# Kernel tuning notes

Measured on AMD Instinct MI355X. Metric: run time of the kernel, lower is better.

The kernel has to match this reference:

```python
import jax, jax.numpy as jnp
import numpy as np
from jax import lax

GAMMA = 1.0

def _conv(x, w, b, stride, pad):
    y = lax.conv_general_dilated(x, w, (stride, stride), [(pad, pad), (pad, pad)],
                                 dimension_numbers=('NCHW', 'OIHW', 'NCHW'))
    return y + b[None, :, None, None]

def _maxpool2s1(x):
    return lax.reduce_window(x, -jnp.inf, lax.max, (1, 1, 2, 2), (1, 1, 1, 1), 'VALID')

def setup_inputs() -> dict:
    key = jax.random.key(0)
    ks = jax.random.split(key, 13)
    d = {}
    d['x'] = jax.random.normal(ks[0], (128, 3, 250, 250), dtype=jnp.float32)
    d['conv1_w'] = jax.random.normal(ks[1], (6, 3, 5, 5), dtype=jnp.float32) / np.sqrt(3 * 25)
    d['conv1_b'] = jax.random.normal(ks[2], (6,), dtype=jnp.float32) * 0.01
    d['conv2_w'] = jax.random.normal(ks[3], (15, 6, 3, 3), dtype=jnp.float32) / np.sqrt(6 * 9)
    d['conv2_b'] = jax.random.normal(ks[4], (15,), dtype=jnp.float32) * 0.01
    d['fc1_w'] = jax.random.normal(ks[5], (120, 55815), dtype=jnp.float32) / np.sqrt(55815.0)
    d['fc1_b'] = jax.random.normal(ks[6], (120,), dtype=jnp.float32) * 0.01
    d['fc2_w'] = jax.random.normal(ks[7], (84, 120), dtype=jnp.float32) / np.sqrt(120.0)
    d['fc2_b'] = jax.random.normal(ks[8], (84,), dtype=jnp.float32) * 0.01
    d['fc3_w'] = jax.random.normal(ks[9], (1, 84), dtype=jnp.float32) / np.sqrt(84.0)
    d['fc3_b'] = jax.random.normal(ks[10], (1,), dtype=jnp.float32) * 0.01
    d['support'] = jax.random.normal(ks[11], (10, 1), dtype=jnp.float32)
    return d

def reference(x, conv1_w, conv1_b, conv2_w, conv2_b, fc1_w, fc1_b, fc2_w, fc2_b, fc3_w, fc3_b, support):
    h = jax.nn.relu(_conv(x, conv1_w, conv1_b, 2, 1))   # [B,6,124,124]
    h = _maxpool2s1(h)                                   # [B,6,123,123] (dropout = identity in eval)
    h = jax.nn.relu(_conv(h, conv2_w, conv2_b, 2, 1))    # [B,15,62,62]
    h = _maxpool2s1(h)                                   # [B,15,61,61]
    h = h.reshape(h.shape[0], -1)                        # [B,55815]
    h = jax.nn.relu(h @ fc1_w.T + fc1_b)
    h = jax.nn.relu(h @ fc2_w.T + fc2_b)
    h = h @ fc3_w.T + fc3_b                              # [B,1]
    # fused RBF kernel vs support set: k[i,j] = exp(-gamma*(x_i - s_j)^2)
    diff = h - support[:, 0][None, :]                    # [B,10]
    k = jnp.exp(-GAMMA * diff * diff)
    h = k.mean(axis=1, keepdims=True)                    # [B,1]
    probs = jax.nn.sigmoid(h)
    return jnp.concatenate((probs, 1.0 - probs), axis=-1)  # [B,2]
```

## Files before the change

### kernel.cpp

```cpp
#include <hip/hip_runtime.h>
#include <math.h>


#define BATCH 128

#define C1_ST 150
#define C1_TOT (37 * 133)
__global__ __launch_bounds__(256) void conv1_pool_kernel(
    const float* __restrict__ x, const float* __restrict__ w,
    const float* __restrict__ bias, float* __restrict__ out) {
  const int b = blockIdx.z;
  const int P0 = blockIdx.x * 64;
  const int R0 = blockIdx.y * 16;
  const int tid = threadIdx.x;
  const int t = tid >> 4;
  const int s = tid & 15;

  __shared__ float lds[37 * C1_ST];

  float acc0[5][6], acc1[5][6];
#pragma unroll
  for (int oc = 0; oc < 6; oc++) {
    float bv = bias[oc];
#pragma unroll
    for (int dc = 0; dc < 5; dc++) { acc0[dc][oc] = bv; acc1[dc][oc] = bv; }
  }

  const int ihb = 2 * R0 - 1, iwb = 2 * P0 - 1;

#pragma unroll 1
  for (int ci = 0; ci < 3; ci++) {
    __syncthreads();
    const float* src = x + (size_t)(b * 3 + ci) * 62500;
#pragma unroll 1
    for (int base = tid; base < C1_TOT; base += 2048) {
      float vv[8];
      int lrv[8], ilv[8];
#pragma unroll
      for (int k = 0; k < 8; k++) {
        int i = base + (k << 8);
        int lr = (int)(((unsigned)i * 63073u) >> 23);
        int il = i - lr * 133;
        lrv[k] = lr; ilv[k] = il;
        int ih = ihb + lr, iw = iwb + il;
        bool ok = (i < C1_TOT) && ((unsigned)ih < 250u) && ((unsigned)iw < 250u);
        vv[k] = ok ? src[ih * 250 + iw] : 0.f;
      }
#pragma unroll
      for (int k = 0; k < 8; k++) {
        int i = base + (k << 8);
        if (i < C1_TOT) lds[lrv[k] * C1_ST + ilv[k] + (ilv[k] >> 3)] = vv[k];
      }
    }
    __syncthreads();

#pragma unroll 1
    for (int ir = 0; ir < 7; ir++) {
      const float* rp = &lds[(2 * t + ir) * C1_ST + 9 * s];
      float v[13];
#pragma unroll
      for (int j = 0; j < 13; j++) v[j] = rp[j + (j >> 3)];

      if (ir < 5) {
#pragma unroll
        for (int oc = 0; oc < 6; oc++) {
          const float* wr = w + ((oc * 3 + ci) * 5 + ir) * 5;
          float w0 = wr[0], w1 = wr[1], w2 = wr[2], w3 = wr[3], w4 = wr[4];
#pragma unroll
          for (int dc = 0; dc < 5; dc++) {
            float a = acc0[dc][oc];
            a += w0 * v[2 * dc + 0];
            a += w1 * v[2 * dc + 1];
            a += w2 * v[2 * dc + 2];
            a += w3 * v[2 * dc + 3];
            a += w4 * v[2 * dc + 4];
            acc0[dc][oc] = a;
          }
        }
      }
      if (ir >= 2) {
#pragma unroll
        for (int oc = 0; oc < 6; oc++) {
          const float* wr = w + ((oc * 3 + ci) * 5 + (ir - 2)) * 5;
          float w0 = wr[0], w1 = wr[1], w2 = wr[2], w3 = wr[3], w4 = wr[4];
#pragma unroll
          for (int dc = 0; dc < 5; dc++) {
            float a = acc1[dc][oc];
            a += w0 * v[2 * dc + 0];
            a += w1 * v[2 * dc + 1];
            a += w2 * v[2 * dc + 2];
            a += w3 * v[2 * dc + 3];
            a += w4 * v[2 * dc + 4];
            acc1[dc][oc] = a;
          }
        }
      }
    }
  }

  const int r = R0 + t;
  const int c0 = P0 + 4 * s;
  if (r < 123) {
#pragma unroll
    for (int oc = 0; oc < 6; oc++) {
      float* orow = out + ((size_t)(b * 6 + oc) * 123 + r) * 123;
      float m0 = fmaxf(fmaxf(fmaxf(acc0[0][oc], acc0[1][oc]),
                             fmaxf(acc1[0][oc], acc1[1][oc])), 0.f);
      float m1 = fmaxf(fmaxf(fmaxf(acc0[1][oc], acc0[2][oc]),
                             fmaxf(acc1[1][oc], acc1[2][oc])), 0.f);
      float m2 = fmaxf(fmaxf(fmaxf(acc0[2][oc], acc0[3][oc]),
                             fmaxf(acc1[2][oc], acc1[3][oc])), 0.f);
      float m3 = fmaxf(fmaxf(fmaxf(acc0[3][oc], acc0[4][oc]),
                             fmaxf(acc1[3][oc], acc1[4][oc])), 0.f);
      if (c0 + 3 < 123) {
        float4 st = make_float4(m0, m1, m2, m3);
        *(float4*)&orow[c0] = st;
      } else {
        if (c0 < 123) orow[c0] = m0;
        if (c0 + 1 < 123) orow[c0 + 1] = m1;
        if (c0 + 2 < 123) orow[c0 + 2] = m2;
      }
    }
  }
}

#define C2_ST 84
#define C2_TOT (35 * 67)
__global__ __launch_bounds__(256) void conv2_pool_kernel(
    const float* __restrict__ in, const float* __restrict__ w,
    const float* __restrict__ bias, float* __restrict__ out) {
  const int b = blockIdx.z;
  const int P0 = blockIdx.x * 32;
  const int R0 = blockIdx.y * 16;
  const int tid = threadIdx.x;
  const int t = tid >> 4;
  const int s = tid & 15;

  __shared__ float lds[35 * C2_ST];

  const int ihb = 2 * R0 - 1, iwb = 2 * P0 - 1;
  const int r = R0 + t;
  const int c0 = P0 + 2 * s;

#pragma unroll 1
  for (int ocg = 0; ocg < 2; ocg++) {
    const int oc0 = ocg * 7;
    float acc0[3][8], acc1[3][8];
#pragma unroll
    for (int k = 0; k < 8; k++) {
      float bv = bias[oc0 + k];
#pragma unroll
      for (int dc = 0; dc < 3; dc++) { acc0[dc][k] = bv; acc1[dc][k] = bv; }
    }

#pragma unroll 1
    for (int ci = 0; ci < 6; ci++) {
      __syncthreads();
      const float* src = in + (size_t)(b * 6 + ci) * 15129;
#pragma unroll 1
      for (int base = tid; base < C2_TOT; base += 2048) {
        float vv[8];
        int lrv[8], ilv[8];
#pragma unroll
        for (int k = 0; k < 8; k++) {
          int i = base + (k << 8);
          int lr = (int)(((unsigned)i * 125204u) >> 23);
          int il = i - lr * 67;
          lrv[k] = lr; ilv[k] = il;
          int ih = ihb + lr, iw = iwb + il;
          bool ok = (i < C2_TOT) && ((unsigned)ih < 123u) && ((unsigned)iw < 123u);
          vv[k] = ok ? src[ih * 123 + iw] : 0.f;
        }
#pragma unroll
        for (int k = 0; k < 8; k++) {
          int i = base + (k << 8);
          if (i < C2_TOT) lds[lrv[k] * C2_ST + ilv[k] + (ilv[k] >> 2)] = vv[k];
        }
      }
      __syncthreads();

#pragma unroll 1
      for (int ir = 0; ir < 5; ir++) {
        const float* rp = &lds[(2 * t + ir) * C2_ST + 5 * s];
        float v[7];
#pragma unroll
        for (int j = 0; j < 7; j++) v[j] = rp[j + (j >> 2)];

        if (ir < 3) {
#pragma unroll
          for (int k = 0; k < 8; k++) {
            const float* wr = w + (((oc0 + k) * 6 + ci) * 3 + ir) * 3;
            float w0 = wr[0], w1 = wr[1], w2 = wr[2];
#pragma unroll
            for (int dc = 0; dc < 3; dc++) {
              float a = acc0[dc][k];
              a += w0 * v[2 * dc + 0];
              a += w1 * v[2 * dc + 1];
              a += w2 * v[2 * dc + 2];
              acc0[dc][k] = a;
            }
          }
        }
        if (ir >= 2) {
#pragma unroll
          for (int k = 0; k < 8; k++) {
            const float* wr = w + (((oc0 + k) * 6 + ci) * 3 + (ir - 2)) * 3;
            float w0 = wr[0], w1 = wr[1], w2 = wr[2];
#pragma unroll
            for (int dc = 0; dc < 3; dc++) {
              float a = acc1[dc][k];
              a += w0 * v[2 * dc + 0];
              a += w1 * v[2 * dc + 1];
              a += w2 * v[2 * dc + 2];
              acc1[dc][k] = a;
            }
          }
        }
      }
    }

    if (r < 61) {
#pragma unroll
      for (int k = 0; k < 8; k++) {
        int oc = oc0 + k;
        float* orow = out + ((size_t)(b * 15 + oc) * 61 + r) * 61;
        float m0 = fmaxf(fmaxf(fmaxf(acc0[0][k], acc0[1][k]),
                               fmaxf(acc1[0][k], acc1[1][k])), 0.f);
        float m1 = fmaxf(fmaxf(fmaxf(acc0[1][k], acc0[2][k]),
                               fmaxf(acc1[1][k], acc1[2][k])), 0.f);
        if (c0 + 1 < 61) {
          float2 st = make_float2(m0, m1);
          *(float2*)&orow[c0] = st;
        } else if (c0 < 61) {
          orow[c0] = m0;
        }
      }
    }
  }
}

#define KTOT 55815
#define NPART 512
#define KCHUNK 112
__global__ __launch_bounds__(512) void fc1_splitk_kernel(
    const float* __restrict__ act, const float* __restrict__ w,
    float* __restrict__ partial) {
  const int kbase = blockIdx.x * KCHUNK;
  const int tid = threadIdx.x;
  const int tx = tid & 31, ty = tid >> 5;
  __shared__ float ldsA[8 * 132];
  __shared__ float ldsB[8 * 132];
  float acc[8][4];
#pragma unroll
  for (int i = 0; i < 8; i++)
#pragma unroll
    for (int j = 0; j < 4; j++) acc[i][j] = 0.f;

  for (int s8 = 0; s8 < KCHUNK / 8; s8++) {
    int kofs = kbase + s8 * 8;
    __syncthreads();
    for (int i = tid; i < 1024; i += 512) {
      int m = i >> 3, kk = i & 7;
      int k = kofs + kk;
      ldsA[kk * 132 + m] = (k < KTOT) ? act[m * KTOT + k] : 0.f;
    }
    for (int i = tid; i < 960; i += 512) {
      int n = i >> 3, kk = i & 7;
      int k = kofs + kk;
      ldsB[kk * 132 + n] = (k < KTOT) ? w[n * KTOT + k] : 0.f;
    }
    __syncthreads();
#pragma unroll
    for (int kk = 0; kk < 8; kk++) {
      float4 a0 = *(const float4*)&ldsA[kk * 132 + ty * 8];
      float4 a1 = *(const float4*)&ldsA[kk * 132 + ty * 8 + 4];
      float4 b0 = *(const float4*)&ldsB[kk * 132 + tx * 4];
      float av[8] = {a0.x, a0.y, a0.z, a0.w, a1.x, a1.y, a1.z, a1.w};
      float bv[4] = {b0.x, b0.y, b0.z, b0.w};
#pragma unroll
      for (int i = 0; i < 8; i++)
#pragma unroll
        for (int j = 0; j < 4; j++) acc[i][j] += av[i] * bv[j];
    }
  }

  if (tx < 30) {
    float* dst = partial + (size_t)blockIdx.x * 15360;
#pragma unroll
    for (int i = 0; i < 8; i++) {
      int row = ty * 8 + i;
      float4 st = make_float4(acc[i][0], acc[i][1], acc[i][2], acc[i][3]);
      *(float4*)&dst[row * 120 + tx * 4] = st;
    }
  }
}

__global__ __launch_bounds__(64) void fc1_reduce1_kernel(
    const float* __restrict__ partial, float* __restrict__ partial2) {
  int idx = blockIdx.x * 64 + threadIdx.x;
  int g = blockIdx.y;
  const float* p = partial + (size_t)g * 64 * 15360 + idx;
  float s = 0.f;
#pragma unroll 8
  for (int q = 0; q < 64; q++) s += p[(size_t)q * 15360];
  partial2[(size_t)g * 15360 + idx] = s;
}

__global__ __launch_bounds__(64) void fc1_reduce2_kernel(
    const float* __restrict__ partial2, const float* __restrict__ bias,
    float* __restrict__ h1) {
  int idx = blockIdx.x * 64 + threadIdx.x;
  float s = 0.f;
#pragma unroll
  for (int g = 0; g < 8; g++) s += partial2[(size_t)g * 15360 + idx];
  h1[idx] = fmaxf(s + bias[idx % 120], 0.f);
}

__global__ __launch_bounds__(128) void head_kernel(
    const float* __restrict__ h1, const float* __restrict__ fc2_w,
    const float* __restrict__ fc2_b, const float* __restrict__ fc3_w,
    const float* __restrict__ fc3_b, const float* __restrict__ support,
    float* __restrict__ out) {
  int b = blockIdx.x, t = threadIdx.x;
  __shared__ float hrow[120];
  __shared__ float s2[84];
  if (t < 120) hrow[t] = h1[b * 120 + t];
  __syncthreads();
  if (t < 84) {
    float d = fc2_b[t];
    for (int k = 0; k < 120; k++) d += fc2_w[t * 120 + k] * hrow[k];
    s2[t] = fmaxf(d, 0.f);
  }
  __syncthreads();
  if (t == 0) {
    float h = fc3_b[0];
    for (int j = 0; j < 84; j++) h += fc3_w[j] * s2[j];
    float ks = 0.f;
    for (int j = 0; j < 10; j++) {
      float diff = h - support[j];
      ks += expf(-diff * diff);
    }
    ks *= 0.1f;
    float p = 1.f / (1.f + expf(-ks));
    out[b * 2] = p;
    out[b * 2 + 1] = 1.f - p;
  }
}

extern "C" void kernel_launch(void* const* d_in, const int* in_sizes, int n_in,
                              void* d_out, int out_size, void* d_ws, size_t ws_size,
                              hipStream_t stream) {
  const float* x   = (const float*)d_in[0];
  const float* c1w = (const float*)d_in[1];
  const float* c1b = (const float*)d_in[2];
  const float* c2w = (const float*)d_in[3];
  const float* c2b = (const float*)d_in[4];
  const float* f1w = (const float*)d_in[5];
  const float* f1b = (const float*)d_in[6];
  const float* f2w = (const float*)d_in[7];
  const float* f2b = (const float*)d_in[8];
  const float* f3w = (const float*)d_in[9];
  const float* f3b = (const float*)d_in[10];
  const float* sup = (const float*)d_in[11];
  float* out = (float*)d_out;

  char* ws = (char*)d_ws;
  float* pool1 = (float*)ws;
  float* act   = (float*)(ws + 46476288);
  float* part  = (float*)ws;
  float* h1    = (float*)(ws + 33000000);
  float* part2 = (float*)(ws + 34000000);

  conv1_pool_kernel<<<dim3(2, 8, BATCH), 256, 0, stream>>>(x, c1w, c1b, pool1);
  conv2_pool_kernel<<<dim3(2, 4, BATCH), 256, 0, stream>>>(pool1, c2w, c2b, act);
  fc1_splitk_kernel<<<NPART, 512, 0, stream>>>(act, f1w, part);
  fc1_reduce1_kernel<<<dim3(240, 8), 64, 0, stream>>>(part, part2);
  fc1_reduce2_kernel<<<240, 64, 0, stream>>>(part2, f1b, h1);
  head_kernel<<<BATCH, 128, 0, stream>>>(h1, f2w, f2b, f3w, f3b, sup, out);
}
```

Measured before the change: 360.7 us.

## Share conv rows between pool outputs in conv1 via LDS exchange

conv1 is re-tiled so that each thread produces two pooled output rows (stride 2 in pool rows) instead of one. The second row reuses the neighbouring thread's acc0 values, exchanged through LDS, which removes the redundant conv row computation that the stride-1 2x2 pool caused. Tiles become 31 rows by 32 columns with 128 threads, and the input halo is reshaped to match. The cost is an extra LDS exchange with barriers and a smaller block size.

```diff
diff --git a/kernel.cpp b/kernel.cpp
--- a/kernel.cpp
+++ b/kernel.cpp
@@ -4,19 +4,22 @@
 
 #define BATCH 128
 
-#define C1_ST 150
-#define C1_TOT (37 * 133)
-__global__ __launch_bounds__(256) void conv1_pool_kernel(
+#define C1_ST 82
+#define C1_COLS 69
+#define C1_ROWS 67
+#define C1_TOT (C1_ROWS * C1_COLS)
+__global__ __launch_bounds__(128) void conv1_pool_kernel(
     const float* __restrict__ x, const float* __restrict__ w,
     const float* __restrict__ bias, float* __restrict__ out) {
   const int b = blockIdx.z;
-  const int P0 = blockIdx.x * 64;
-  const int R0 = blockIdx.y * 16;
+  const int P0 = blockIdx.x * 32;
+  const int R0 = blockIdx.y * 31;
   const int tid = threadIdx.x;
-  const int t = tid >> 4;
-  const int s = tid & 15;
-
-  __shared__ float lds[37 * C1_ST];
+  const int t = tid >> 3;
+  const int s = tid & 7;
+
+  __shared__ float lds[C1_ROWS * C1_ST];
+  float* cbuf = lds;
 
   float acc0[5][6], acc1[5][6];
 #pragma unroll
@@ -33,14 +36,14 @@
     __syncthreads();
     const float* src = x + (size_t)(b * 3 + ci) * 62500;
 #pragma unroll 1
-    for (int base = tid; base < C1_TOT; base += 2048) {
+    for (int base = tid; base < C1_TOT; base += 1024) {
       float vv[8];
       int lrv[8], ilv[8];
 #pragma unroll
       for (int k = 0; k < 8; k++) {
-        int i = base + (k << 8);
-        int lr = (int)(((unsigned)i * 63073u) >> 23);
-        int il = i - lr * 133;
+        int i = base + (k << 7);
+        int lr = (int)(((unsigned)i * 121575u) >> 23);
+        int il = i - lr * 69;
         lrv[k] = lr; ilv[k] = il;
         int ih = ihb + lr, iw = iwb + il;
         bool ok = (i < C1_TOT) && ((unsigned)ih < 250u) && ((unsigned)iw < 250u);
@@ -48,7 +51,7 @@
       }
 #pragma unroll
       for (int k = 0; k < 8; k++) {
-        int i = base + (k << 8);
+        int i = base + (k << 7);
         if (i < C1_TOT) lds[lrv[k] * C1_ST + ilv[k] + (ilv[k] >> 3)] = vv[k];
       }
     }
@@ -56,7 +59,7 @@
 
 #pragma unroll 1
     for (int ir = 0; ir < 7; ir++) {
-      const float* rp = &lds[(2 * t + ir) * C1_ST + 9 * s];
+      const float* rp = &lds[(4 * t + ir) * C1_ST + 9 * s];
       float v[13];
 #pragma unroll
       for (int j = 0; j < 13; j++) v[j] = rp[j + (j >> 3)];
@@ -98,12 +101,19 @@
     }
   }
 
-  const int r = R0 + t;
+  __syncthreads();
+#pragma unroll
+  for (int oc = 0; oc < 6; oc++)
+#pragma unroll
+    for (int dc = 0; dc < 5; dc++)
+      cbuf[tid * 31 + oc * 5 + dc] = acc0[dc][oc];
+
+  const int p0 = R0 + 2 * t;
   const int c0 = P0 + 4 * s;
-  if (r < 123) {
+  if (p0 < 123) {
 #pragma unroll
     for (int oc = 0; oc < 6; oc++) {
-      float* orow = out + ((size_t)(b * 6 + oc) * 123 + r) * 123;
+      float* orow = out + ((size_t)(b * 6 + oc) * 123 + p0) * 123;
       float m0 = fmaxf(fmaxf(fmaxf(acc0[0][oc], acc0[1][oc]),
                              fmaxf(acc1[0][oc], acc1[1][oc])), 0.f);
       float m1 = fmaxf(fmaxf(fmaxf(acc0[1][oc], acc0[2][oc]),
@@ -113,8 +123,29 @@
       float m3 = fmaxf(fmaxf(fmaxf(acc0[3][oc], acc0[4][oc]),
                              fmaxf(acc1[3][oc], acc1[4][oc])), 0.f);
       if (c0 + 3 < 123) {
-        float4 st = make_float4(m0, m1, m2, m3);
-        *(float4*)&orow[c0] = st;
+        *(float4*)&orow[c0] = make_float4(m0, m1, m2, m3);
+      } else {
+        if (c0 < 123) orow[c0] = m0;
+        if (c0 + 1 < 123) orow[c0 + 1] = m1;
+        if (c0 + 2 < 123) orow[c0 + 2] = m2;
+      }
+    }
+  }
+
+  __syncthreads();
+  if (t < 15 && p0 + 1 < 123) {
+    const float* nb = &cbuf[(tid + 8) * 31];
+#pragma unroll
+    for (int oc = 0; oc < 6; oc++) {
+      float n0 = nb[oc * 5 + 0], n1 = nb[oc * 5 + 1], n2 = nb[oc * 5 + 2];
+      float n3 = nb[oc * 5 + 3], n4 = nb[oc * 5 + 4];
+      float* orow = out + ((size_t)(b * 6 + oc) * 123 + p0 + 1) * 123;
+      float m0 = fmaxf(fmaxf(fmaxf(acc1[0][oc], acc1[1][oc]), fmaxf(n0, n1)), 0.f);
+      float m1 = fmaxf(fmaxf(fmaxf(acc1[1][oc], acc1[2][oc]), fmaxf(n1, n2)), 0.f);
+      float m2 = fmaxf(fmaxf(fmaxf(acc1[2][oc], acc1[3][oc]), fmaxf(n2, n3)), 0.f);
+      float m3 = fmaxf(fmaxf(fmaxf(acc1[3][oc], acc1[4][oc]), fmaxf(n3, n4)), 0.f);
+      if (c0 + 3 < 123) {
+        *(float4*)&orow[c0] = make_float4(m0, m1, m2, m3);
       } else {
         if (c0 < 123) orow[c0] = m0;
         if (c0 + 1 < 123) orow[c0 + 1] = m1;
@@ -229,8 +260,7 @@
         float m1 = fmaxf(fmaxf(fmaxf(acc0[1][k], acc0[2][k]),
                                fmaxf(acc1[1][k], acc1[2][k])), 0.f);
         if (c0 + 1 < 61) {
-          float2 st = make_float2(m0, m1);
-          *(float2*)&orow[c0] = st;
+          *(float2*)&orow[c0] = make_float2(m0, m1);
         } else if (c0 < 61) {
           orow[c0] = m0;
         }
@@ -371,7 +401,7 @@
   float* h1    = (float*)(ws + 33000000);
   float* part2 = (float*)(ws + 34000000);
 
-  conv1_pool_kernel<<<dim3(2, 8, BATCH), 256, 0, stream>>>(x, c1w, c1b, pool1);
+  conv1_pool_kernel<<<dim3(4, 4, BATCH), 128, 0, stream>>>(x, c1w, c1b, pool1);
   conv2_pool_kernel<<<dim3(2, 4, BATCH), 256, 0, stream>>>(pool1, c2w, c2b, act);
   fc1_splitk_kernel<<<NPART, 512, 0, stream>>>(act, f1w, part);
   fc1_reduce1_kernel<<<dim3(240, 8), 64, 0, stream>>>(part, part2);
```

New measurement: 359.3 us. About the same (-0.4%).
